# Performance work log

Hardware: AMD Instinct MI355X
Metric: run time of the kernel (lower is better)

The kernel has to match this reference:

```python
import jax, jax.numpy as jnp
import numpy as np

WIN = 7  # window size (w1 = w2 = 7)

def _rel_pos_indices(w: int) -> jnp.ndarray:
    # Matches RelPosBias 2-D branch: [(w*w), (w*w)] indices into (2w-1)^2 table
    p = np.arange(w)
    gi, gj = np.meshgrid(p, p, indexing='ij')
    grid = np.stack([gi.reshape(-1), gj.reshape(-1)], axis=-1)  # [w*w, 2]
    rel = grid[:, None, :] - grid[None, :, :]                   # [w*w, w*w, 2]
    rel = rel + (w - 1)
    idx = rel[..., 0] * (2 * w - 1) + rel[..., 1]               # [w*w, w*w]
    return jnp.asarray(idx, dtype=jnp.int32)


def setup_inputs() -> dict:
    key = jax.random.key(0)
    k1, k2, k3, k4 = jax.random.split(key, 4)
    dim, heads = 256, 8
    b, gx, gy = 64, 8, 8
    x = jax.random.normal(k1, (b, gx, gy, WIN, WIN, dim), dtype=jnp.float32)
    # torch nn.Linear weight layout: [out_features, in_features]
    w_qkv = jax.random.normal(k2, (3 * dim, dim), dtype=jnp.float32) * (dim ** -0.5)
    w_out = jax.random.normal(k3, (dim, dim), dtype=jnp.float32) * (dim ** -0.5)
    rel_emb = jax.random.normal(k4, ((2 * WIN - 1) ** 2, heads), dtype=jnp.float32) * 0.02
    rel_idx = _rel_pos_indices(WIN)
    return {"x": x, "w_qkv": w_qkv, "w_out": w_out, "rel_emb": rel_emb, "rel_idx": rel_idx}


def reference(x, w_qkv, w_out, rel_emb, rel_idx):
    b, gx, gy, w1, w2, d = x.shape
    h = rel_emb.shape[1]          # heads
    dh = d // h                    # dim_head
    scale = dh ** -0.5
    n = w1 * w2                    # tokens per window (49)

    xr = x.reshape(b * gx * gy, n, d)                        # (B, n, d)
    qkv = jnp.einsum('bnd,ed->bne', xr, w_qkv)               # (B, n, 3d)
    q, k, v = jnp.split(qkv, 3, axis=-1)
    split_heads = lambda t: t.reshape(t.shape[0], n, h, dh).transpose(0, 2, 1, 3)
    q, k, v = map(split_heads, (q, k, v))                    # (B, h, n, dh)

    sim = jnp.einsum('bhid,bhjd->bhij', q * scale, k)        # (B, h, n, n)
    bias = rel_emb[rel_idx]                                   # (n, n, h)
    sim = sim + bias.transpose(2, 0, 1)[None]                 # + (1, h, n, n)
    attn = jax.nn.softmax(sim, axis=-1)

    out = jnp.einsum('bhij,bhjd->bhid', attn, v)              # (B, h, n, dh)
    out = out.transpose(0, 2, 1, 3).reshape(-1, w1, w2, d)    # (B, w1, w2, d)
    out = jnp.einsum('bxyd,ed->bxye', out, w_out)
    return out.reshape(b, gx, gy, w1, w2, d)
```

## Files before the change

kernel.cpp:

```cpp
#include <hip/hip_runtime.h>
#include <hip/hip_bf16.h>

typedef __bf16 bf16x8 __attribute__((ext_vector_type(8)));
typedef __bf16 bf16x4v __attribute__((ext_vector_type(4)));
typedef float f32x4 __attribute__((ext_vector_type(4)));

#define MFMA(a, b, c) __builtin_amdgcn_mfma_f32_16x16x32_bf16((a), (b), (c), 0, 0, 0)
#define NEG_BIG (-1e30f)

#define XO_LD 264
#define W_LD 136
#define QK_LD 36
#define VT_LD 72
#define P_LD 68
#define OTR_LD 36

#define WR_ELS (96 * W_LD)
#define P_OFF 0
#define OTR_OFF (64 * P_LD)
#define Q_OFF WR_ELS
#define K_OFF (Q_OFF + 64 * QK_LD)
#define VT_OFF (K_OFF + 64 * QK_LD)
#define TOTAL_ELS (VT_OFF + 32 * VT_LD)

static __device__ inline bf16x8 ld8x2(const __bf16* p) {
  bf16x4v lo = *(const bf16x4v*)p;
  bf16x4v hi = *(const bf16x4v*)(p + 4);
  bf16x8 r;
  r[0] = lo[0]; r[1] = lo[1]; r[2] = lo[2]; r[3] = lo[3];
  r[4] = hi[0]; r[5] = hi[1]; r[6] = hi[2]; r[7] = hi[3];
  return r;
}

__global__ __launch_bounds__(256) void prep_kernel(
    const float* __restrict__ w_qkv, const float* __restrict__ w_out,
    const float* __restrict__ rel_emb, const int* __restrict__ rel_idx,
    __bf16* __restrict__ wqkv_b, __bf16* __restrict__ wout_b,
    float* __restrict__ bias) {
  const float kScale = 0.17677669529663687f;
  int idx = blockIdx.x * 256 + threadIdx.x;
  if (idx < 196608) {
    float v = w_qkv[idx];
    if (idx < 65536) v *= kScale;
    wqkv_b[idx] = (__bf16)v;
  } else if (idx < 262144) {
    int j = idx - 196608;
    wout_b[j] = (__bf16)w_out[j];
  } else if (idx < 294912) {
    int j = idx - 262144;
    int h = j >> 12, i = (j >> 6) & 63, c = j & 63;
    float v = NEG_BIG;
    if (i < 49 && c < 49) v = rel_emb[rel_idx[i * 49 + c] * 8 + h];
    bias[j] = v;
  }
}

__global__ __launch_bounds__(256, 4) void attn_kernel(
    const float* __restrict__ x, const __bf16* __restrict__ wqkv,
    const __bf16* __restrict__ wout, const float* __restrict__ bias,
    float* __restrict__ out) {
  __shared__ __attribute__((aligned(16))) __bf16 sm[TOTAL_ELS];

  const int tid = threadIdx.x;
  const int wave = tid >> 6;
  const int lane = tid & 63;
  const int quad = lane >> 4;
  const int l16 = lane & 15;
  const int i0 = wave * 16 + quad * 4;
  const int am = wave * 16 + l16;

  const f32x4 fzero = {0.f, 0.f, 0.f, 0.f};

  {
    const float4* xg = (const float4*)(x + (size_t)blockIdx.x * 12544);
    for (int i = tid; i < 3136; i += 256) {
      float4 v = xg[i];
      int row = i >> 6, c4 = (i & 63) << 2;
      bf16x4v t;
      t[0] = (__bf16)v.x; t[1] = (__bf16)v.y; t[2] = (__bf16)v.z; t[3] = (__bf16)v.w;
      *(bf16x4v*)&sm[row * XO_LD + c4] = t;
    }
    bf16x4v z;
    z[0] = z[1] = z[2] = z[3] = (__bf16)0.0f;
    for (int i = tid; i < 960; i += 256) {
      int row = 49 + (i >> 6), c4 = (i & 63) << 2;
      *(bf16x4v*)&sm[row * XO_LD + c4] = z;
    }
  }
  __syncthreads();

  bf16x8 afr[8];
#pragma unroll
  for (int kk = 0; kk < 8; ++kk)
    afr[kk] = *(const bf16x8*)&sm[am * XO_LD + kk * 32 + quad * 8];

  bf16x8 ofr[8];

  for (int h = 0; h < 8; ++h) {
    f32x4 acc[6];
#pragma unroll
    for (int t = 0; t < 6; ++t) acc[t] = fzero;

#pragma unroll
    for (int kh = 0; kh < 2; ++kh) {
      __syncthreads();
      for (int i = tid; i < 1536; i += 256) {
        int lr = i >> 4, c = (i & 15) * 8;
        int grow = (lr >> 5) * 256 + h * 32 + (lr & 31);
        *(bf16x8*)&sm[lr * W_LD + c] =
            *(const bf16x8*)&wqkv[grow * 256 + kh * 128 + c];
      }
      __syncthreads();
#pragma unroll
      for (int k2 = 0; k2 < 4; ++k2) {
        bf16x8 a = afr[kh * 4 + k2];
#pragma unroll
        for (int t = 0; t < 6; ++t) {
          bf16x8 b = *(const bf16x8*)&sm[(t * 16 + l16) * W_LD + k2 * 32 + quad * 8];
          acc[t] = MFMA(a, b, acc[t]);
        }
      }
    }

    f32x4 sim[4];
    {
      const float* bb = bias + (h << 12);
#pragma unroll
      for (int nt = 0; nt < 4; ++nt)
#pragma unroll
        for (int r = 0; r < 4; ++r) sim[nt][r] = bb[(i0 + r) * 64 + nt * 16 + l16];
    }

#pragma unroll
    for (int t = 0; t < 2; ++t) {
#pragma unroll
      for (int r = 0; r < 4; ++r) {
        sm[Q_OFF + (i0 + r) * QK_LD + t * 16 + l16] = (__bf16)acc[t][r];
        sm[K_OFF + (i0 + r) * QK_LD + t * 16 + l16] = (__bf16)acc[2 + t][r];
      }
      bf16x4v pv;
#pragma unroll
      for (int r = 0; r < 4; ++r) pv[r] = (__bf16)acc[4 + t][r];
      *(bf16x4v*)&sm[VT_OFF + (t * 16 + l16) * VT_LD + i0] = pv;
    }
    __syncthreads();

    {
      bf16x8 a = ld8x2(&sm[Q_OFF + am * QK_LD + quad * 8]);
#pragma unroll
      for (int nt = 0; nt < 4; ++nt) {
        bf16x8 b = ld8x2(&sm[K_OFF + (nt * 16 + l16) * QK_LD + quad * 8]);
        sim[nt] = MFMA(a, b, sim[nt]);
      }
    }

#pragma unroll
    for (int r = 0; r < 4; ++r) {
      float mx = fmaxf(fmaxf(sim[0][r], sim[1][r]), fmaxf(sim[2][r], sim[3][r]));
      mx = fmaxf(mx, __shfl_xor(mx, 1));
      mx = fmaxf(mx, __shfl_xor(mx, 2));
      mx = fmaxf(mx, __shfl_xor(mx, 4));
      mx = fmaxf(mx, __shfl_xor(mx, 8));
      float e0 = __expf(sim[0][r] - mx), e1 = __expf(sim[1][r] - mx);
      float e2 = __expf(sim[2][r] - mx), e3 = __expf(sim[3][r] - mx);
      float sum = e0 + e1 + e2 + e3;
      sum += __shfl_xor(sum, 1);
      sum += __shfl_xor(sum, 2);
      sum += __shfl_xor(sum, 4);
      sum += __shfl_xor(sum, 8);
      float rs = 1.0f / sum;
      int row = i0 + r;
      sm[P_OFF + row * P_LD + l16] = (__bf16)(e0 * rs);
      sm[P_OFF + row * P_LD + 16 + l16] = (__bf16)(e1 * rs);
      sm[P_OFF + row * P_LD + 32 + l16] = (__bf16)(e2 * rs);
      sm[P_OFF + row * P_LD + 48 + l16] = (__bf16)(e3 * rs);
    }
    __syncthreads();

    f32x4 oa[2];
    oa[0] = fzero;
    oa[1] = fzero;
#pragma unroll
    for (int kk = 0; kk < 2; ++kk) {
      bf16x8 a = ld8x2(&sm[P_OFF + am * P_LD + kk * 32 + quad * 8]);
#pragma unroll
      for (int t = 0; t < 2; ++t) {
        bf16x8 b = *(const bf16x8*)&sm[VT_OFF + (t * 16 + l16) * VT_LD + kk * 32 + quad * 8];
        oa[t] = MFMA(a, b, oa[t]);
      }
    }
#pragma unroll
    for (int t = 0; t < 2; ++t)
#pragma unroll
      for (int r = 0; r < 4; ++r)
        sm[OTR_OFF + (i0 + r) * OTR_LD + t * 16 + l16] = (__bf16)oa[t][r];
    __syncthreads();
    ofr[h] = ld8x2(&sm[OTR_OFF + am * OTR_LD + quad * 8]);
  }

  for (int rr = 0; rr < 4; ++rr) {
    __syncthreads();
    for (int i = tid; i < 2048; i += 256) {
      int lr = i >> 5, c = (i & 31) * 8;
      *(bf16x8*)&sm[lr * XO_LD + c] = *(const bf16x8*)&wout[(rr * 64 + lr) * 256 + c];
    }
    __syncthreads();
#pragma unroll
    for (int e2 = 0; e2 < 2; ++e2) {
      f32x4 fa[2];
      fa[0] = fzero;
      fa[1] = fzero;
#pragma unroll
      for (int kk = 0; kk < 8; ++kk) {
        bf16x8 a = ofr[kk];
#pragma unroll
        for (int t = 0; t < 2; ++t) {
          bf16x8 b = *(const bf16x8*)&sm[(e2 * 32 + t * 16 + l16) * XO_LD + kk * 32 + quad * 8];
          fa[t] = MFMA(a, b, fa[t]);
        }
      }
      float* ob = out + (size_t)blockIdx.x * 12544 + (rr * 2 + e2) * 32;
#pragma unroll
      for (int t = 0; t < 2; ++t)
#pragma unroll
        for (int r = 0; r < 4; ++r) {
          int row = i0 + r;
          if (row < 49) ob[row * 256 + t * 16 + l16] = fa[t][r];
        }
    }
  }
}

extern "C" void kernel_launch(void* const* d_in, const int* in_sizes, int n_in,
                              void* d_out, int out_size, void* d_ws, size_t ws_size,
                              hipStream_t stream) {
  (void)in_sizes; (void)n_in; (void)out_size; (void)ws_size;
  const float* x = (const float*)d_in[0];
  const float* w_qkv = (const float*)d_in[1];
  const float* w_out = (const float*)d_in[2];
  const float* rel_emb = (const float*)d_in[3];
  const int* rel_idx = (const int*)d_in[4];
  float* out = (float*)d_out;

  char* ws = (char*)d_ws;
  __bf16* wqkv_b = (__bf16*)ws;
  __bf16* wout_b = (__bf16*)(ws + 393216);
  float* bias = (float*)(ws + 524288);

  prep_kernel<<<1152, 256, 0, stream>>>(w_qkv, w_out, rel_emb, rel_idx,
                                        wqkv_b, wout_b, bias);
  attn_kernel<<<4096, 256, 0, stream>>>(x, wqkv_b, wout_b, bias, out);
}
```

Baseline: 845.8 us.

## Assign two heads per wave and drop block-wide syncs in attention loop

Each wave now owns two attention heads and computes all 64 rows for them, so the per-head loop needs no block barriers and uses private per-wave LDS for Q, K, V^T and P. QKV weights and x are read straight from global memory into MFMA fragments, with x converted from fp32 each time, instead of being staged through shared memory. The bias table is stored pre-swizzled in MFMA accumulator order so it can be loaded as vectors. In exchange, register pressure rises a lot (launch bounds drop to two blocks per SM), x is re-read from global once per head, and head outputs are exchanged through a single LDS transpose before the output projection.

Measured after the change: 1.517 ms. +79.4%, slower.

```diff
diff --git a/kernel.cpp b/kernel.cpp
--- a/kernel.cpp
+++ b/kernel.cpp
@@ -8,20 +8,13 @@
 #define MFMA(a, b, c) __builtin_amdgcn_mfma_f32_16x16x32_bf16((a), (b), (c), 0, 0, 0)
 #define NEG_BIG (-1e30f)
 
-#define XO_LD 264
-#define W_LD 136
 #define QK_LD 36
 #define VT_LD 72
 #define P_LD 68
-#define OTR_LD 36
-
-#define WR_ELS (96 * W_LD)
-#define P_OFF 0
-#define OTR_OFF (64 * P_LD)
-#define Q_OFF WR_ELS
-#define K_OFF (Q_OFF + 64 * QK_LD)
-#define VT_OFF (K_OFF + 64 * QK_LD)
-#define TOTAL_ELS (VT_OFF + 32 * VT_LD)
+#define OTR_LD 268
+#define XO_LD 264
+#define WAVE_ELS (2304 + 2304 + 2304)
+#define TOTAL_ELS (4 * WAVE_ELS)
 
 static __device__ inline bf16x8 ld8x2(const __bf16* p) {
   bf16x4v lo = *(const bf16x4v*)p;
@@ -48,14 +41,20 @@
     wout_b[j] = (__bf16)w_out[j];
   } else if (idx < 294912) {
     int j = idx - 262144;
-    int h = j >> 12, i = (j >> 6) & 63, c = j & 63;
+    int h = j >> 12;
+    int mt = (j >> 10) & 3;
+    int nt = (j >> 8) & 3;
+    int lane = (j >> 2) & 63;
+    int r = j & 3;
+    int row = mt * 16 + ((lane >> 4) << 2) + r;
+    int col = nt * 16 + (lane & 15);
     float v = NEG_BIG;
-    if (i < 49 && c < 49) v = rel_emb[rel_idx[i * 49 + c] * 8 + h];
+    if (row < 49 && col < 49) v = rel_emb[rel_idx[row * 49 + col] * 8 + h];
     bias[j] = v;
   }
 }
 
-__global__ __launch_bounds__(256, 4) void attn_kernel(
+__global__ __launch_bounds__(256, 2) void attn_kernel(
     const float* __restrict__ x, const __bf16* __restrict__ wqkv,
     const __bf16* __restrict__ wout, const float* __restrict__ bias,
     float* __restrict__ out) {
@@ -70,133 +69,147 @@
   const int am = wave * 16 + l16;
 
   const f32x4 fzero = {0.f, 0.f, 0.f, 0.f};
-
-  {
-    const float4* xg = (const float4*)(x + (size_t)blockIdx.x * 12544);
-    for (int i = tid; i < 3136; i += 256) {
-      float4 v = xg[i];
-      int row = i >> 6, c4 = (i & 63) << 2;
-      bf16x4v t;
-      t[0] = (__bf16)v.x; t[1] = (__bf16)v.y; t[2] = (__bf16)v.z; t[3] = (__bf16)v.w;
-      *(bf16x4v*)&sm[row * XO_LD + c4] = t;
-    }
-    bf16x4v z;
-    z[0] = z[1] = z[2] = z[3] = (__bf16)0.0f;
-    for (int i = tid; i < 960; i += 256) {
-      int row = 49 + (i >> 6), c4 = (i & 63) << 2;
-      *(bf16x4v*)&sm[row * XO_LD + c4] = z;
-    }
-  }
+  const float* xg = x + (size_t)blockIdx.x * 12544;
+
+  __bf16* mq = sm + wave * WAVE_ELS;
+  __bf16* mk = mq + 2304;
+  __bf16* mv = mk + 2304;
+  __bf16* mp = mq;
+
+  f32x4 oacc[2][4][2];
+
+#pragma unroll
+  for (int hh = 0; hh < 2; ++hh) {
+    const int h = wave * 2 + hh;
+
+    f32x4 acc[4][6];
+#pragma unroll
+    for (int mt = 0; mt < 4; ++mt)
+#pragma unroll
+      for (int nt = 0; nt < 6; ++nt) acc[mt][nt] = fzero;
+
+#pragma unroll
+    for (int k2 = 0; k2 < 8; ++k2) {
+      bf16x8 b[6];
+#pragma unroll
+      for (int nt = 0; nt < 6; ++nt) {
+        int grow = (nt >> 1) * 256 + h * 32 + (nt & 1) * 16 + l16;
+        b[nt] = *(const bf16x8*)&wqkv[grow * 256 + k2 * 32 + quad * 8];
+      }
+#pragma unroll
+      for (int mt = 0; mt < 4; ++mt) {
+        int xr = mt * 16 + l16;
+        if (xr > 48) xr = 48;
+        const float* xp = xg + xr * 256 + k2 * 32 + quad * 8;
+        float4 v0 = *(const float4*)xp;
+        float4 v1 = *(const float4*)(xp + 4);
+        bf16x8 a;
+        a[0] = (__bf16)v0.x; a[1] = (__bf16)v0.y; a[2] = (__bf16)v0.z; a[3] = (__bf16)v0.w;
+        a[4] = (__bf16)v1.x; a[5] = (__bf16)v1.y; a[6] = (__bf16)v1.z; a[7] = (__bf16)v1.w;
+#pragma unroll
+        for (int nt = 0; nt < 6; ++nt) acc[mt][nt] = MFMA(a, b[nt], acc[mt][nt]);
+      }
+    }
+
+#pragma unroll
+    for (int mt = 0; mt < 4; ++mt) {
+      int row = mt * 16 + quad * 4;
+#pragma unroll
+      for (int t = 0; t < 2; ++t) {
+#pragma unroll
+        for (int r = 0; r < 4; ++r) {
+          mq[(row + r) * QK_LD + t * 16 + l16] = (__bf16)acc[mt][t][r];
+          mk[(row + r) * QK_LD + t * 16 + l16] = (__bf16)acc[mt][2 + t][r];
+        }
+        bf16x4v pv;
+#pragma unroll
+        for (int r = 0; r < 4; ++r) pv[r] = (__bf16)acc[mt][4 + t][r];
+        *(bf16x4v*)&mv[(t * 16 + l16) * VT_LD + row] = pv;
+      }
+    }
+
+    f32x4 sim[4][4];
+    const float* bb = bias + (h << 12) + (lane << 2);
+#pragma unroll
+    for (int mt = 0; mt < 4; ++mt)
+#pragma unroll
+      for (int nt = 0; nt < 4; ++nt)
+        sim[mt][nt] = *(const f32x4*)&bb[(mt * 4 + nt) << 8];
+
+    bf16x8 aq[4];
+#pragma unroll
+    for (int mt = 0; mt < 4; ++mt)
+      aq[mt] = ld8x2(&mq[(mt * 16 + l16) * QK_LD + quad * 8]);
+#pragma unroll
+    for (int nt = 0; nt < 4; ++nt) {
+      bf16x8 bk = ld8x2(&mk[(nt * 16 + l16) * QK_LD + quad * 8]);
+#pragma unroll
+      for (int mt = 0; mt < 4; ++mt) sim[mt][nt] = MFMA(aq[mt], bk, sim[mt][nt]);
+    }
+
+#pragma unroll
+    for (int mt = 0; mt < 4; ++mt) {
+#pragma unroll
+      for (int r = 0; r < 4; ++r) {
+        float mx = fmaxf(fmaxf(sim[mt][0][r], sim[mt][1][r]),
+                         fmaxf(sim[mt][2][r], sim[mt][3][r]));
+        mx = fmaxf(mx, __shfl_xor(mx, 1));
+        mx = fmaxf(mx, __shfl_xor(mx, 2));
+        mx = fmaxf(mx, __shfl_xor(mx, 4));
+        mx = fmaxf(mx, __shfl_xor(mx, 8));
+        float e0 = __expf(sim[mt][0][r] - mx), e1 = __expf(sim[mt][1][r] - mx);
+        float e2 = __expf(sim[mt][2][r] - mx), e3 = __expf(sim[mt][3][r] - mx);
+        float sum = e0 + e1 + e2 + e3;
+        sum += __shfl_xor(sum, 1);
+        sum += __shfl_xor(sum, 2);
+        sum += __shfl_xor(sum, 4);
+        sum += __shfl_xor(sum, 8);
+        float rs = 1.0f / sum;
+        int row = mt * 16 + quad * 4 + r;
+        mp[row * P_LD + l16] = (__bf16)(e0 * rs);
+        mp[row * P_LD + 16 + l16] = (__bf16)(e1 * rs);
+        mp[row * P_LD + 32 + l16] = (__bf16)(e2 * rs);
+        mp[row * P_LD + 48 + l16] = (__bf16)(e3 * rs);
+      }
+    }
+
+#pragma unroll
+    for (int mt = 0; mt < 4; ++mt)
+#pragma unroll
+      for (int t = 0; t < 2; ++t) oacc[hh][mt][t] = fzero;
+#pragma unroll
+    for (int kk = 0; kk < 2; ++kk) {
+      bf16x8 bv[2];
+#pragma unroll
+      for (int t = 0; t < 2; ++t)
+        bv[t] = *(const bf16x8*)&mv[(t * 16 + l16) * VT_LD + kk * 32 + quad * 8];
+#pragma unroll
+      for (int mt = 0; mt < 4; ++mt) {
+        bf16x8 ap = ld8x2(&mp[(mt * 16 + l16) * P_LD + kk * 32 + quad * 8]);
+#pragma unroll
+        for (int t = 0; t < 2; ++t) oacc[hh][mt][t] = MFMA(ap, bv[t], oacc[hh][mt][t]);
+      }
+    }
+  }
+
   __syncthreads();
-
-  bf16x8 afr[8];
-#pragma unroll
-  for (int kk = 0; kk < 8; ++kk)
-    afr[kk] = *(const bf16x8*)&sm[am * XO_LD + kk * 32 + quad * 8];
-
+#pragma unroll
+  for (int hh = 0; hh < 2; ++hh) {
+    int cb = (wave * 2 + hh) * 32;
+#pragma unroll
+    for (int mt = 0; mt < 4; ++mt)
+#pragma unroll
+      for (int t = 0; t < 2; ++t)
+#pragma unroll
+        for (int r = 0; r < 4; ++r)
+          sm[(mt * 16 + quad * 4 + r) * OTR_LD + cb + t * 16 + l16] =
+              (__bf16)oacc[hh][mt][t][r];
+  }
+  __syncthreads();
   bf16x8 ofr[8];
-
-  for (int h = 0; h < 8; ++h) {
-    f32x4 acc[6];
-#pragma unroll
-    for (int t = 0; t < 6; ++t) acc[t] = fzero;
-
-#pragma unroll
-    for (int kh = 0; kh < 2; ++kh) {
-      __syncthreads();
-      for (int i = tid; i < 1536; i += 256) {
-        int lr = i >> 4, c = (i & 15) * 8;
-        int grow = (lr >> 5) * 256 + h * 32 + (lr & 31);
-        *(bf16x8*)&sm[lr * W_LD + c] =
-            *(const bf16x8*)&wqkv[grow * 256 + kh * 128 + c];
-      }
-      __syncthreads();
-#pragma unroll
-      for (int k2 = 0; k2 < 4; ++k2) {
-        bf16x8 a = afr[kh * 4 + k2];
-#pragma unroll
-        for (int t = 0; t < 6; ++t) {
-          bf16x8 b = *(const bf16x8*)&sm[(t * 16 + l16) * W_LD + k2 * 32 + quad * 8];
-          acc[t] = MFMA(a, b, acc[t]);
-        }
-      }
-    }
-
-    f32x4 sim[4];
-    {
-      const float* bb = bias + (h << 12);
-#pragma unroll
-      for (int nt = 0; nt < 4; ++nt)
-#pragma unroll
-        for (int r = 0; r < 4; ++r) sim[nt][r] = bb[(i0 + r) * 64 + nt * 16 + l16];
-    }
-
-#pragma unroll
-    for (int t = 0; t < 2; ++t) {
-#pragma unroll
-      for (int r = 0; r < 4; ++r) {
-        sm[Q_OFF + (i0 + r) * QK_LD + t * 16 + l16] = (__bf16)acc[t][r];
-        sm[K_OFF + (i0 + r) * QK_LD + t * 16 + l16] = (__bf16)acc[2 + t][r];
-      }
-      bf16x4v pv;
-#pragma unroll
-      for (int r = 0; r < 4; ++r) pv[r] = (__bf16)acc[4 + t][r];
-      *(bf16x4v*)&sm[VT_OFF + (t * 16 + l16) * VT_LD + i0] = pv;
-    }
-    __syncthreads();
-
-    {
-      bf16x8 a = ld8x2(&sm[Q_OFF + am * QK_LD + quad * 8]);
-#pragma unroll
-      for (int nt = 0; nt < 4; ++nt) {
-        bf16x8 b = ld8x2(&sm[K_OFF + (nt * 16 + l16) * QK_LD + quad * 8]);
-        sim[nt] = MFMA(a, b, sim[nt]);
-      }
-    }
-
-#pragma unroll
-    for (int r = 0; r < 4; ++r) {
-      float mx = fmaxf(fmaxf(sim[0][r], sim[1][r]), fmaxf(sim[2][r], sim[3][r]));
-      mx = fmaxf(mx, __shfl_xor(mx, 1));
-      mx = fmaxf(mx, __shfl_xor(mx, 2));
-      mx = fmaxf(mx, __shfl_xor(mx, 4));
-      mx = fmaxf(mx, __shfl_xor(mx, 8));
-      float e0 = __expf(sim[0][r] - mx), e1 = __expf(sim[1][r] - mx);
-      float e2 = __expf(sim[2][r] - mx), e3 = __expf(sim[3][r] - mx);
-      float sum = e0 + e1 + e2 + e3;
-      sum += __shfl_xor(sum, 1);
-      sum += __shfl_xor(sum, 2);
-      sum += __shfl_xor(sum, 4);
-      sum += __shfl_xor(sum, 8);
-      float rs = 1.0f / sum;
-      int row = i0 + r;
-      sm[P_OFF + row * P_LD + l16] = (__bf16)(e0 * rs);
-      sm[P_OFF + row * P_LD + 16 + l16] = (__bf16)(e1 * rs);
-      sm[P_OFF + row * P_LD + 32 + l16] = (__bf16)(e2 * rs);
-      sm[P_OFF + row * P_LD + 48 + l16] = (__bf16)(e3 * rs);
-    }
-    __syncthreads();
-
-    f32x4 oa[2];
-    oa[0] = fzero;
-    oa[1] = fzero;
-#pragma unroll
-    for (int kk = 0; kk < 2; ++kk) {
-      bf16x8 a = ld8x2(&sm[P_OFF + am * P_LD + kk * 32 + quad * 8]);
-#pragma unroll
-      for (int t = 0; t < 2; ++t) {
-        bf16x8 b = *(const bf16x8*)&sm[VT_OFF + (t * 16 + l16) * VT_LD + kk * 32 + quad * 8];
-        oa[t] = MFMA(a, b, oa[t]);
-      }
-    }
-#pragma unroll
-    for (int t = 0; t < 2; ++t)
-#pragma unroll
-      for (int r = 0; r < 4; ++r)
-        sm[OTR_OFF + (i0 + r) * OTR_LD + t * 16 + l16] = (__bf16)oa[t][r];
-    __syncthreads();
-    ofr[h] = ld8x2(&sm[OTR_OFF + am * OTR_LD + quad * 8]);
-  }
+#pragma unroll
+  for (int k8 = 0; k8 < 8; ++k8)
+    ofr[k8] = ld8x2(&sm[am * OTR_LD + k8 * 32 + quad * 8]);
 
   for (int rr = 0; rr < 4; ++rr) {
     __syncthreads();
@@ -212,11 +225,10 @@
       fa[1] = fzero;
 #pragma unroll
       for (int kk = 0; kk < 8; ++kk) {
-        bf16x8 a = ofr[kk];
 #pragma unroll
         for (int t = 0; t < 2; ++t) {
-          bf16x8 b = *(const bf16x8*)&sm[(e2 * 32 + t * 16 + l16) * XO_LD + kk * 32 + quad * 8];
-          fa[t] = MFMA(a, b, fa[t]);
+          bf16x8 bw = *(const bf16x8*)&sm[(e2 * 32 + t * 16 + l16) * XO_LD + kk * 32 + quad * 8];
+          fa[t] = MFMA(ofr[kk], bw, fa[t]);
         }
       }
       float* ob = out + (size_t)blockIdx.x * 12544 + (rr * 2 + e2) * 32;
```

## Pre-swizzle weights and bias into MFMA fragment order, load B operands from global

Applied to the files above, without the earlier changes.

The prep kernel now writes the QKV and output-projection weights, and the relative-position bias, in the exact per-lane MFMA fragment layout. The attention kernel then reads each B fragment directly from global memory (through the cache) as one contiguous 16-byte load per lane. This removes the per-head LDS staging of the weights and their __syncthreads barriers, and the LDS footprint shrinks to the x tile. The risk is more global/L2 traffic per block, since every block re-reads the weights from cache instead of from shared memory, and the latency of those loads is exposed.

New measurement: 894.5 us. +5.8%, slower.

```diff
diff --git a/kernel.cpp b/kernel.cpp
--- a/kernel.cpp
+++ b/kernel.cpp
@@ -9,19 +9,16 @@
 #define NEG_BIG (-1e30f)
 
 #define XO_LD 264
-#define W_LD 136
 #define QK_LD 36
 #define VT_LD 72
 #define P_LD 68
 #define OTR_LD 36
-
-#define WR_ELS (96 * W_LD)
-#define P_OFF 0
-#define OTR_OFF (64 * P_LD)
-#define Q_OFF WR_ELS
-#define K_OFF (Q_OFF + 64 * QK_LD)
-#define VT_OFF (K_OFF + 64 * QK_LD)
-#define TOTAL_ELS (VT_OFF + 32 * VT_LD)
+#define Q_OFF 0
+#define K_OFF 2304
+#define VT_OFF 4608
+#define P_OFF 6912
+#define OTR_OFF 11264
+#define TOTAL_ELS (64 * XO_LD)
 
 static __device__ inline bf16x8 ld8x2(const __bf16* p) {
   bf16x4v lo = *(const bf16x4v*)p;
@@ -35,22 +32,42 @@
 __global__ __launch_bounds__(256) void prep_kernel(
     const float* __restrict__ w_qkv, const float* __restrict__ w_out,
     const float* __restrict__ rel_emb, const int* __restrict__ rel_idx,
-    __bf16* __restrict__ wqkv_b, __bf16* __restrict__ wout_b,
+    __bf16* __restrict__ wqkv_f, __bf16* __restrict__ wout_f,
     float* __restrict__ bias) {
   const float kScale = 0.17677669529663687f;
   int idx = blockIdx.x * 256 + threadIdx.x;
-  if (idx < 196608) {
-    float v = w_qkv[idx];
-    if (idx < 65536) v *= kScale;
-    wqkv_b[idx] = (__bf16)v;
-  } else if (idx < 262144) {
-    int j = idx - 196608;
-    wout_b[j] = (__bf16)w_out[j];
-  } else if (idx < 294912) {
-    int j = idx - 262144;
-    int h = j >> 12, i = (j >> 6) & 63, c = j & 63;
+  if (idx < 24576) {
+    int lane = idx & 63, k2 = (idx >> 6) & 7;
+    int hn = idx >> 9;
+    int nt = hn % 6, h = hn / 6;
+    int quad = lane >> 4, l16 = lane & 15;
+    int grow = (nt >> 1) * 256 + h * 32 + (nt & 1) * 16 + l16;
+    const float* src = w_qkv + grow * 256 + k2 * 32 + quad * 8;
+    float s = (nt < 2) ? kScale : 1.0f;
+    bf16x8 d;
+#pragma unroll
+    for (int j = 0; j < 8; ++j) d[j] = (__bf16)(src[j] * s);
+    *(bf16x8*)&wqkv_f[idx * 8] = d;
+  } else if (idx < 32768) {
+    int j2 = idx - 24576;
+    int lane = j2 & 63, kk = (j2 >> 6) & 7, ntile = j2 >> 9;
+    int quad = lane >> 4, l16 = lane & 15;
+    const float* src = w_out + (ntile * 16 + l16) * 256 + kk * 32 + quad * 8;
+    bf16x8 d;
+#pragma unroll
+    for (int j = 0; j < 8; ++j) d[j] = (__bf16)src[j];
+    *(bf16x8*)&wout_f[j2 * 8] = d;
+  } else if (idx < 65536) {
+    int j = idx - 32768;
+    int h = j >> 12;
+    int mt = (j >> 10) & 3;
+    int nt = (j >> 8) & 3;
+    int lane = (j >> 2) & 63;
+    int r = j & 3;
+    int row = mt * 16 + ((lane >> 4) << 2) + r;
+    int col = nt * 16 + (lane & 15);
     float v = NEG_BIG;
-    if (i < 49 && c < 49) v = rel_emb[rel_idx[i * 49 + c] * 8 + h];
+    if (row < 49 && col < 49) v = rel_emb[rel_idx[row * 49 + col] * 8 + h];
     bias[j] = v;
   }
 }
@@ -93,6 +110,7 @@
 #pragma unroll
   for (int kk = 0; kk < 8; ++kk)
     afr[kk] = *(const bf16x8*)&sm[am * XO_LD + kk * 32 + quad * 8];
+  __syncthreads();
 
   bf16x8 ofr[8];
 
@@ -100,35 +118,24 @@
     f32x4 acc[6];
 #pragma unroll
     for (int t = 0; t < 6; ++t) acc[t] = fzero;
-
-#pragma unroll
-    for (int kh = 0; kh < 2; ++kh) {
-      __syncthreads();
-      for (int i = tid; i < 1536; i += 256) {
-        int lr = i >> 4, c = (i & 15) * 8;
-        int grow = (lr >> 5) * 256 + h * 32 + (lr & 31);
-        *(bf16x8*)&sm[lr * W_LD + c] =
-            *(const bf16x8*)&wqkv[grow * 256 + kh * 128 + c];
-      }
-      __syncthreads();
-#pragma unroll
-      for (int k2 = 0; k2 < 4; ++k2) {
-        bf16x8 a = afr[kh * 4 + k2];
-#pragma unroll
-        for (int t = 0; t < 6; ++t) {
-          bf16x8 b = *(const bf16x8*)&sm[(t * 16 + l16) * W_LD + k2 * 32 + quad * 8];
-          acc[t] = MFMA(a, b, acc[t]);
+    {
+      const __bf16* wb = wqkv + (size_t)h * 24576;
+#pragma unroll
+      for (int k2 = 0; k2 < 8; ++k2) {
+        bf16x8 a = afr[k2];
+#pragma unroll
+        for (int nt = 0; nt < 6; ++nt) {
+          bf16x8 b = *(const bf16x8*)&wb[(nt * 8 + k2) * 512 + lane * 8];
+          acc[nt] = MFMA(a, b, acc[nt]);
         }
       }
     }
 
     f32x4 sim[4];
     {
-      const float* bb = bias + (h << 12);
-#pragma unroll
-      for (int nt = 0; nt < 4; ++nt)
-#pragma unroll
-        for (int r = 0; r < 4; ++r) sim[nt][r] = bb[(i0 + r) * 64 + nt * 16 + l16];
+      const float* bb = bias + (h << 12) + (wave << 10) + (lane << 2);
+#pragma unroll
+      for (int nt = 0; nt < 4; ++nt) sim[nt] = *(const f32x4*)&bb[nt << 8];
     }
 
 #pragma unroll
@@ -198,36 +205,27 @@
     ofr[h] = ld8x2(&sm[OTR_OFF + am * OTR_LD + quad * 8]);
   }
 
-  for (int rr = 0; rr < 4; ++rr) {
-    __syncthreads();
-    for (int i = tid; i < 2048; i += 256) {
-      int lr = i >> 5, c = (i & 31) * 8;
-      *(bf16x8*)&sm[lr * XO_LD + c] = *(const bf16x8*)&wout[(rr * 64 + lr) * 256 + c];
-    }
-    __syncthreads();
-#pragma unroll
-    for (int e2 = 0; e2 < 2; ++e2) {
-      f32x4 fa[2];
-      fa[0] = fzero;
-      fa[1] = fzero;
-#pragma unroll
-      for (int kk = 0; kk < 8; ++kk) {
-        bf16x8 a = ofr[kk];
-#pragma unroll
-        for (int t = 0; t < 2; ++t) {
-          bf16x8 b = *(const bf16x8*)&sm[(e2 * 32 + t * 16 + l16) * XO_LD + kk * 32 + quad * 8];
-          fa[t] = MFMA(a, b, fa[t]);
-        }
-      }
-      float* ob = out + (size_t)blockIdx.x * 12544 + (rr * 2 + e2) * 32;
-#pragma unroll
-      for (int t = 0; t < 2; ++t)
-#pragma unroll
-        for (int r = 0; r < 4; ++r) {
-          int row = i0 + r;
-          if (row < 49) ob[row * 256 + t * 16 + l16] = fa[t][r];
-        }
-    }
+  float* ob_base = out + (size_t)blockIdx.x * 12544;
+  for (int ct = 0; ct < 8; ++ct) {
+    f32x4 fa[2];
+    fa[0] = fzero;
+    fa[1] = fzero;
+#pragma unroll
+    for (int kk = 0; kk < 8; ++kk) {
+#pragma unroll
+      for (int t = 0; t < 2; ++t) {
+        bf16x8 bw = *(const bf16x8*)&wout[((ct * 2 + t) * 8 + kk) * 512 + lane * 8];
+        fa[t] = MFMA(ofr[kk], bw, fa[t]);
+      }
+    }
+    float* ob = ob_base + ct * 32;
+#pragma unroll
+    for (int t = 0; t < 2; ++t)
+#pragma unroll
+      for (int r = 0; r < 4; ++r) {
+        int row = i0 + r;
+        if (row < 49) ob[row * 256 + t * 16 + l16] = fa[t][r];
+      }
   }
 }
 
@@ -243,11 +241,11 @@
   float* out = (float*)d_out;
 
   char* ws = (char*)d_ws;
-  __bf16* wqkv_b = (__bf16*)ws;
-  __bf16* wout_b = (__bf16*)(ws + 393216);
+  __bf16* wqkv_f = (__bf16*)ws;
+  __bf16* wout_f = (__bf16*)(ws + 393216);
   float* bias = (float*)(ws + 524288);
 
-  prep_kernel<<<1152, 256, 0, stream>>>(w_qkv, w_out, rel_emb, rel_idx,
-                                        wqkv_b, wout_b, bias);
-  attn_kernel<<<4096, 256, 0, stream>>>(x, wqkv_b, wout_b, bias, out);
-}
+  prep_kernel<<<256, 256, 0, stream>>>(w_qkv, w_out, rel_emb, rel_idx,
+                                       wqkv_f, wout_f, bias);
+  attn_kernel<<<4096, 256, 0, stream>>>(x, wqkv_f, wout_f, bias, out);
+}
```
